# Optimization experiments

Measured on AMD Instinct MI355X. Metric: run time of the kernel, lower is better.

## Reference

```python
import jax, jax.numpy as jnp
import numpy as np

N, D, H = 500000, 128, 128
B, M = 1024, 512


def setup_inputs() -> dict:
    key = jax.random.key(0)
    k = jax.random.split(key, 8)
    return {
        "embed": jax.random.normal(k[0], (N, D), dtype=jnp.float32),
        "node_feat": jax.random.normal(k[1], (N, D), dtype=jnp.float32),
        "W1": jax.random.normal(k[2], (2 * D, H), dtype=jnp.float32) * 0.05,
        "b1": jnp.zeros((H,), dtype=jnp.float32),
        "W2": jax.random.normal(k[3], (H, 1), dtype=jnp.float32) * 0.05,
        "b2": jnp.zeros((1,), dtype=jnp.float32),
        "query_idx": jax.random.randint(k[4], (B,), 0, N),
        "cand_idx": jax.random.randint(k[5], (B, M), 0, N),
        "top_k": 3,
    }


def reference(embed, node_feat, W1, b1, W2, b2, query_idx, cand_idx, top_k):
    # Gather query and candidate (k-hop subgraph) embeddings.
    q = embed[query_idx]                                   # [B, D]
    c = embed[cand_idx]                                    # [B, M, D]
    Bv, Mv, Dv = c.shape
    pair = jnp.concatenate(
        [jnp.broadcast_to(q[:, None, :], (Bv, Mv, Dv)), c], axis=-1
    )                                                      # [B, M, 2D]
    # Tiny 2-layer MLP edge scorer (one fused pass over all edges).
    h = jax.nn.relu(jnp.einsum("bmf,fh->bmh", pair, W1) + b1)
    scores = (jnp.einsum("bmh,ho->bmo", h, W2) + b2)[..., 0]  # [B, M]
    # Sort-based top-k selection (original sorted per-etype lists).
    _, pos = jax.lax.top_k(scores, top_k)                  # [B, k]
    top_nodes = jnp.take_along_axis(cand_idx, pos, axis=1) # [B, k]
    # Zero out features of the selected nodes (hard mask), as in original.
    masked_feat = node_feat.at[top_nodes.reshape(-1)].set(0.0)
    return scores, masked_feat
```

## Files before the change

### kernel.cpp

```cpp
#include <hip/hip_runtime.h>
#include <math.h>

#define D 128
#define H 128
#define BQ 1024
#define M 512
#define NNODES 500000
#define K_MAX 8
#define SHORT 16
#define NTILE (BQ * M / 64)
#define NCOPY 2048
#define COPY_N4 ((long)NNODES * D / 4)

typedef __attribute__((ext_vector_type(8))) short bf16x8;
typedef __attribute__((ext_vector_type(4))) float f32x4;

static __device__ __forceinline__ unsigned pack2bf(float a, float b) {
    unsigned ua = __float_as_uint(a);
    unsigned ub = __float_as_uint(b);
    ua = ua + 0x7fffu + ((ua >> 16) & 1u);
    ub = ub + 0x7fffu + ((ub >> 16) & 1u);
    return (ua >> 16) | (ub & 0xffff0000u);
}

__global__ void wconv_kernel(const float* __restrict__ W1,
                             unsigned short* __restrict__ wTswz) {
    const int idx = blockIdx.x * 256 + threadIdx.x;
    const int h = idx >> 7;
    const int inner = (idx & 127) * 2;
    const int k = (inner ^ ((h & 7) << 4)) >> 1;
    const float v = W1[(long)(D + k) * H + h];
    wTswz[idx] = (unsigned short)pack2bf(v, 0.f);
}

__global__ void qproj_kernel(const float* __restrict__ embed,
                             const float* __restrict__ W1,
                             const float* __restrict__ b1,
                             const int* __restrict__ query_idx,
                             float* __restrict__ qh) {
    __shared__ float qrow[D];
    const int b = blockIdx.x;
    const int t = threadIdx.x;
    const long qi = query_idx[b];
    qrow[t] = embed[qi * D + t];
    __syncthreads();
    float acc = b1[t];
#pragma unroll 8
    for (int d = 0; d < D; ++d)
        acc = fmaf(qrow[d], W1[d * H + t], acc);
    qh[b * H + t] = acc;
}

__global__ __launch_bounds__(256)
void fused_kernel(const float* __restrict__ embed,
                  const unsigned short* __restrict__ wTswz,
                  const float* __restrict__ W2,
                  const float* __restrict__ b2,
                  const int* __restrict__ cand_idx,
                  const float* __restrict__ qh,
                  float* __restrict__ scores,
                  const f32x4* __restrict__ nf_src,
                  f32x4* __restrict__ nf_dst) {
    __shared__ __align__(16) char smem[16384 + 32768];
    const int bid = blockIdx.x;
    const int t   = threadIdx.x;

    if (bid % 5 == 0) {
        const int cb = bid / 5;
        long i = (long)cb * 256 + t;
        const long stride = (long)NCOPY * 256;
        for (; i < COPY_N4; i += stride) {
            const f32x4 v = __builtin_nontemporal_load(&nf_src[i]);
            __builtin_nontemporal_store(v, &nf_dst[i]);
        }
        return;
    }

    char* As = smem;
    char* Bs = smem + 16384;

    const int tile = bid - bid / 5 - 1;
    const int b   = tile >> 3;
    const int m0  = (tile & 7) * 64;

    {
        const int e = t >> 2;
        const int q = t & 3;
        const long node = cand_idx[b * M + m0 + e];
        const float* rowp = embed + node * D;
        const int sw = (e & 7) << 4;
#pragma unroll
        for (int i = 0; i < 8; ++i) {
            const int c4 = i * 4 + q;
            const f32x4 v = *(const f32x4*)(rowp + c4 * 4);
            uint2 p;
            p.x = pack2bf(v.x, v.y);
            p.y = pack2bf(v.z, v.w);
            *(uint2*)(As + (e << 8) + ((c4 * 8) ^ sw)) = p;
        }
    }
    {
#pragma unroll
        for (int i = 0; i < 8; ++i) {
            const int c = i * 256 + t;
            const uint4 v = ((const uint4*)wTswz)[c];
            *(uint4*)(Bs + (size_t)c * 16) = v;
        }
    }
    __syncthreads();

    const int lane = t & 63;
    const int w    = t >> 6;
    const int g    = lane >> 4;
    const int c    = lane & 15;
    const int sw   = (c & 7) << 4;

    f32x4 acc[8];
#pragma unroll
    for (int cb2 = 0; cb2 < 8; ++cb2) acc[cb2] = (f32x4){0.f, 0.f, 0.f, 0.f};

    const int arow = (w * 16 + c) << 8;
#pragma unroll
    for (int ks = 0; ks < 4; ++ks) {
        const int koff = (ks * 64 + g * 16) ^ sw;
        const bf16x8 a = *(const bf16x8*)(As + arow + koff);
#pragma unroll
        for (int cb2 = 0; cb2 < 8; ++cb2) {
            const bf16x8 bv = *(const bf16x8*)(Bs + ((cb2 * 16 + c) << 8) + koff);
            acc[cb2] = __builtin_amdgcn_mfma_f32_16x16x32_bf16(a, bv, acc[cb2], 0, 0, 0);
        }
    }

    float s0 = 0.f, s1 = 0.f, s2 = 0.f, s3 = 0.f;
#pragma unroll
    for (int cb2 = 0; cb2 < 8; ++cb2) {
        const int hq = cb2 * 16 + c;
        const float qv = qh[b * H + hq];
        const float w2 = W2[hq];
        s0 = fmaf(fmaxf(qv + acc[cb2][0], 0.f), w2, s0);
        s1 = fmaf(fmaxf(qv + acc[cb2][1], 0.f), w2, s1);
        s2 = fmaf(fmaxf(qv + acc[cb2][2], 0.f), w2, s2);
        s3 = fmaf(fmaxf(qv + acc[cb2][3], 0.f), w2, s3);
    }
#pragma unroll
    for (int off = 1; off <= 8; off <<= 1) {
        s0 += __shfl_xor(s0, off);
        s1 += __shfl_xor(s1, off);
        s2 += __shfl_xor(s2, off);
        s3 += __shfl_xor(s3, off);
    }
    if (c == 0) {
        const float b2v = b2[0];
        float* out = scores + b * M + m0 + w * 16 + g * 4;
        out[0] = s0 + b2v;
        out[1] = s1 + b2v;
        out[2] = s2 + b2v;
        out[3] = s3 + b2v;
    }
}

__global__ void topk16_kernel(const float* __restrict__ scores,
                              int* __restrict__ shortpos) {
    const int b = blockIdx.x;
    const int lane = threadIdx.x;
    const float* row = scores + b * M;
    float v[8];
    {
        const float4 x0 = ((const float4*)row)[lane * 2];
        const float4 x1 = ((const float4*)row)[lane * 2 + 1];
        v[0] = x0.x; v[1] = x0.y; v[2] = x0.z; v[3] = x0.w;
        v[4] = x1.x; v[5] = x1.y; v[6] = x1.z; v[7] = x1.w;
    }
    for (int kk = 0; kk < SHORT; ++kk) {
        float bv = v[0];
        int bi = lane * 8;
#pragma unroll
        for (int j = 1; j < 8; ++j)
            if (v[j] > bv) { bv = v[j]; bi = lane * 8 + j; }
#pragma unroll
        for (int off = 32; off >= 1; off >>= 1) {
            const float ov = __shfl_xor(bv, off);
            const int   oi = __shfl_xor(bi, off);
            if (ov > bv || (ov == bv && oi < bi)) { bv = ov; bi = oi; }
        }
        if (lane == 0) shortpos[b * SHORT + kk] = bi;
        if ((bi >> 3) == lane) v[bi & 7] = -3.402823466e38f;
    }
}

__global__ __launch_bounds__(128)
void refine_kernel(const float* __restrict__ embed,
                   const float* __restrict__ W1,
                   const float* __restrict__ W2,
                   const float* __restrict__ qh,
                   const int* __restrict__ cand_idx,
                   const int* __restrict__ shortpos,
                   const int* __restrict__ topk_ptr,
                   int* __restrict__ top_nodes) {
    __shared__ float crows[SHORT][D];
    __shared__ float red[SHORT][D];
    __shared__ int spos[SHORT];
    const int b = blockIdx.x;
    const int t = threadIdx.x;

    if (t < SHORT) spos[t] = shortpos[b * SHORT + t];
    __syncthreads();
    {
        const int cc = t >> 3;
        const int d0 = (t & 7) * 16;
        const long node = cand_idx[b * M + spos[cc]];
        const float4* rp = (const float4*)(embed + node * D);
        float4* wp = (float4*)&crows[cc][d0];
#pragma unroll
        for (int j = 0; j < 4; ++j) wp[j] = rp[d0 / 4 + j];
    }
    __syncthreads();

    float acc[SHORT];
#pragma unroll
    for (int cc = 0; cc < SHORT; ++cc) acc[cc] = 0.f;
    const float* W1bot = W1 + (long)D * H;
    for (int d = 0; d < D; ++d) {
        const float w1v = W1bot[d * H + t];
#pragma unroll
        for (int cc = 0; cc < SHORT; ++cc)
            acc[cc] = fmaf(crows[cc][d], w1v, acc[cc]);
    }
    const float qv = qh[b * H + t];
    const float w2 = W2[t];
#pragma unroll
    for (int cc = 0; cc < SHORT; ++cc)
        red[cc][t] = fmaxf(qv + acc[cc], 0.f) * w2;
    __syncthreads();

    if (t < 64) {
#pragma unroll
        for (int cc = 0; cc < SHORT; ++cc) {
            float v = red[cc][t] + red[cc][t + 64];
#pragma unroll
            for (int off = 32; off >= 1; off >>= 1) v += __shfl_xor(v, off);
            if (t == 0) red[cc][0] = v;
        }
    }
    __syncthreads();

    if (t == 0) {
        int k = *topk_ptr;
        if (k > K_MAX) k = K_MAX;
        unsigned used = 0;
        for (int kk = 0; kk < K_MAX; ++kk) {
            if (kk < k) {
                int best = -1, bpos = 0x7fffffff;
                float bv = 0.f;
                for (int cc = 0; cc < SHORT; ++cc) {
                    if (used & (1u << cc)) continue;
                    const float v = red[cc][0];
                    const int p = spos[cc];
                    if (best < 0 || v > bv || (v == bv && p < bpos)) {
                        best = cc; bv = v; bpos = p;
                    }
                }
                used |= 1u << best;
                top_nodes[b * K_MAX + kk] = cand_idx[b * M + bpos];
            } else {
                top_nodes[b * K_MAX + kk] = -1;
            }
        }
    }
}

__global__ void zero_rows_kernel(const int* __restrict__ top_nodes,
                                 float* __restrict__ masked) {
    const int node = top_nodes[blockIdx.x];
    if (node < 0) return;
    masked[(long)node * D + threadIdx.x] = 0.f;
}

extern "C" void kernel_launch(void* const* d_in, const int* in_sizes, int n_in,
                              void* d_out, int out_size, void* d_ws, size_t ws_size,
                              hipStream_t stream) {
    const float* embed     = (const float*)d_in[0];
    const float* node_feat = (const float*)d_in[1];
    const float* W1        = (const float*)d_in[2];
    const float* b1        = (const float*)d_in[3];
    const float* W2        = (const float*)d_in[4];
    const float* b2        = (const float*)d_in[5];
    const int*   query_idx = (const int*)d_in[6];
    const int*   cand_idx  = (const int*)d_in[7];
    const int*   topk_ptr  = (const int*)d_in[8];

    float* scores = (float*)d_out;
    float* masked = (float*)d_out + (long)BQ * M;

    char* p = (char*)d_ws;
    float*          qh        = (float*)p;          p += (long)BQ * H * 4;
    int*            shortpos  = (int*)p;            p += (long)BQ * SHORT * 4;
    int*            top_nodes = (int*)p;            p += (long)BQ * K_MAX * 4;
    unsigned short* wTswz     = (unsigned short*)p;

    wconv_kernel<<<(H * D) / 256, 256, 0, stream>>>(W1, wTswz);
    qproj_kernel<<<BQ, H, 0, stream>>>(embed, W1, b1, query_idx, qh);

    fused_kernel<<<NTILE + NCOPY, 256, 0, stream>>>(
        embed, wTswz, W2, b2, cand_idx, qh, scores,
        (const f32x4*)node_feat, (f32x4*)masked);

    topk16_kernel<<<BQ, 64, 0, stream>>>(scores, shortpos);
    refine_kernel<<<BQ, 128, 0, stream>>>(embed, W1, W2, qh, cand_idx,
                                          shortpos, topk_ptr, top_nodes);
    zero_rows_kernel<<<BQ * K_MAX, D, 0, stream>>>(top_nodes, masked);
}
```

Baseline: 205.6 us.

## Score one query per block with register-prefetched gathers and amortized W1 staging

```diff
diff --git a/kernel.cpp b/kernel.cpp
--- a/kernel.cpp
+++ b/kernel.cpp
@@ -8,12 +8,14 @@
 #define NNODES 500000
 #define K_MAX 8
 #define SHORT 16
-#define NTILE (BQ * M / 64)
+#define NSCORE BQ
 #define NCOPY 2048
 #define COPY_N4 ((long)NNODES * D / 4)
+#define CSTRIDE ((long)NCOPY * 256)
 
 typedef __attribute__((ext_vector_type(8))) short bf16x8;
 typedef __attribute__((ext_vector_type(4))) float f32x4;
+typedef __attribute__((ext_vector_type(4))) unsigned u32x4;
 
 static __device__ __forceinline__ unsigned pack2bf(float a, float b) {
     unsigned ua = __float_as_uint(a);
@@ -51,7 +53,7 @@
     qh[b * H + t] = acc;
 }
 
-__global__ __launch_bounds__(256)
+__global__ __launch_bounds__(256, 4)
 void fused_kernel(const float* __restrict__ embed,
                   const unsigned short* __restrict__ wTswz,
                   const float* __restrict__ W2,
@@ -61,44 +63,33 @@
                   float* __restrict__ scores,
                   const f32x4* __restrict__ nf_src,
                   f32x4* __restrict__ nf_dst) {
-    __shared__ __align__(16) char smem[16384 + 32768];
+    __shared__ __align__(16) char Bs[32768];
     const int bid = blockIdx.x;
     const int t   = threadIdx.x;
-
-    if (bid % 5 == 0) {
-        const int cb = bid / 5;
-        long i = (long)cb * 256 + t;
-        const long stride = (long)NCOPY * 256;
-        for (; i < COPY_N4; i += stride) {
+    const int r3  = bid % 3;
+
+    if (r3 != 1) {
+        const int cid = (bid / 3) * 2 + (r3 >> 1);
+        long i = (long)cid * 256 + t;
+        for (; i + 3 * CSTRIDE < COPY_N4; i += 4 * CSTRIDE) {
+            const f32x4 v0 = __builtin_nontemporal_load(&nf_src[i]);
+            const f32x4 v1 = __builtin_nontemporal_load(&nf_src[i + CSTRIDE]);
+            const f32x4 v2 = __builtin_nontemporal_load(&nf_src[i + 2 * CSTRIDE]);
+            const f32x4 v3 = __builtin_nontemporal_load(&nf_src[i + 3 * CSTRIDE]);
+            __builtin_nontemporal_store(v0, &nf_dst[i]);
+            __builtin_nontemporal_store(v1, &nf_dst[i + CSTRIDE]);
+            __builtin_nontemporal_store(v2, &nf_dst[i + 2 * CSTRIDE]);
+            __builtin_nontemporal_store(v3, &nf_dst[i + 3 * CSTRIDE]);
+        }
+        for (; i < COPY_N4; i += CSTRIDE) {
             const f32x4 v = __builtin_nontemporal_load(&nf_src[i]);
             __builtin_nontemporal_store(v, &nf_dst[i]);
         }
         return;
     }
 
-    char* As = smem;
-    char* Bs = smem + 16384;
-
-    const int tile = bid - bid / 5 - 1;
-    const int b   = tile >> 3;
-    const int m0  = (tile & 7) * 64;
-
-    {
-        const int e = t >> 2;
-        const int q = t & 3;
-        const long node = cand_idx[b * M + m0 + e];
-        const float* rowp = embed + node * D;
-        const int sw = (e & 7) << 4;
-#pragma unroll
-        for (int i = 0; i < 8; ++i) {
-            const int c4 = i * 4 + q;
-            const f32x4 v = *(const f32x4*)(rowp + c4 * 4);
-            uint2 p;
-            p.x = pack2bf(v.x, v.y);
-            p.y = pack2bf(v.z, v.w);
-            *(uint2*)(As + (e << 8) + ((c4 * 8) ^ sw)) = p;
-        }
-    }
+    const int b = bid / 3;
+
     {
 #pragma unroll
         for (int i = 0; i < 8; ++i) {
@@ -107,7 +98,6 @@
             *(uint4*)(Bs + (size_t)c * 16) = v;
         }
     }
-    __syncthreads();
 
     const int lane = t & 63;
     const int w    = t >> 6;
@@ -115,47 +105,87 @@
     const int c    = lane & 15;
     const int sw   = (c & 7) << 4;
 
-    f32x4 acc[8];
-#pragma unroll
-    for (int cb2 = 0; cb2 < 8; ++cb2) acc[cb2] = (f32x4){0.f, 0.f, 0.f, 0.f};
-
-    const int arow = (w * 16 + c) << 8;
-#pragma unroll
-    for (int ks = 0; ks < 4; ++ks) {
-        const int koff = (ks * 64 + g * 16) ^ sw;
-        const bf16x8 a = *(const bf16x8*)(As + arow + koff);
-#pragma unroll
-        for (int cb2 = 0; cb2 < 8; ++cb2) {
-            const bf16x8 bv = *(const bf16x8*)(Bs + ((cb2 * 16 + c) << 8) + koff);
-            acc[cb2] = __builtin_amdgcn_mfma_f32_16x16x32_bf16(a, bv, acc[cb2], 0, 0, 0);
-        }
-    }
-
-    float s0 = 0.f, s1 = 0.f, s2 = 0.f, s3 = 0.f;
-#pragma unroll
-    for (int cb2 = 0; cb2 < 8; ++cb2) {
-        const int hq = cb2 * 16 + c;
-        const float qv = qh[b * H + hq];
-        const float w2 = W2[hq];
-        s0 = fmaf(fmaxf(qv + acc[cb2][0], 0.f), w2, s0);
-        s1 = fmaf(fmaxf(qv + acc[cb2][1], 0.f), w2, s1);
-        s2 = fmaf(fmaxf(qv + acc[cb2][2], 0.f), w2, s2);
-        s3 = fmaf(fmaxf(qv + acc[cb2][3], 0.f), w2, s3);
-    }
-#pragma unroll
-    for (int off = 1; off <= 8; off <<= 1) {
-        s0 += __shfl_xor(s0, off);
-        s1 += __shfl_xor(s1, off);
-        s2 += __shfl_xor(s2, off);
-        s3 += __shfl_xor(s3, off);
-    }
-    if (c == 0) {
-        const float b2v = b2[0];
-        float* out = scores + b * M + m0 + w * 16 + g * 4;
-        out[0] = s0 + b2v;
-        out[1] = s1 + b2v;
-        out[2] = s2 + b2v;
-        out[3] = s3 + b2v;
+    float qv[8], w2[8];
+#pragma unroll
+    for (int cb = 0; cb < 8; ++cb) {
+        qv[cb] = qh[b * H + cb * 16 + c];
+        w2[cb] = W2[cb * 16 + c];
+    }
+    const float b2v = b2[0];
+
+    int idx[8];
+    const int ibase = b * M + w * 16 + c;
+#pragma unroll
+    for (int mt = 0; mt < 8; ++mt) idx[mt] = cand_idx[ibase + mt * 64];
+
+    __syncthreads();
+
+    f32x4 buf[8];
+    {
+        const float* rp = embed + (long)idx[0] * D + g * 8;
+#pragma unroll
+        for (int ks = 0; ks < 4; ++ks) {
+            buf[2 * ks]     = *(const f32x4*)(rp + ks * 32);
+            buf[2 * ks + 1] = *(const f32x4*)(rp + ks * 32 + 4);
+        }
+    }
+
+#pragma unroll
+    for (int mt = 0; mt < 8; ++mt) {
+        bf16x8 afr[4];
+#pragma unroll
+        for (int ks = 0; ks < 4; ++ks) {
+            u32x4 u;
+            u.x = pack2bf(buf[2 * ks].x, buf[2 * ks].y);
+            u.y = pack2bf(buf[2 * ks].z, buf[2 * ks].w);
+            u.z = pack2bf(buf[2 * ks + 1].x, buf[2 * ks + 1].y);
+            u.w = pack2bf(buf[2 * ks + 1].z, buf[2 * ks + 1].w);
+            afr[ks] = __builtin_bit_cast(bf16x8, u);
+        }
+        if (mt < 7) {
+            const float* rp = embed + (long)idx[mt + 1] * D + g * 8;
+#pragma unroll
+            for (int ks = 0; ks < 4; ++ks) {
+                buf[2 * ks]     = *(const f32x4*)(rp + ks * 32);
+                buf[2 * ks + 1] = *(const f32x4*)(rp + ks * 32 + 4);
+            }
+        }
+
+        f32x4 acc[8];
+#pragma unroll
+        for (int cb = 0; cb < 8; ++cb) acc[cb] = (f32x4){0.f, 0.f, 0.f, 0.f};
+#pragma unroll
+        for (int ks = 0; ks < 4; ++ks) {
+            const int koff = (ks * 64 + g * 16) ^ sw;
+#pragma unroll
+            for (int cb = 0; cb < 8; ++cb) {
+                const bf16x8 bv = *(const bf16x8*)(Bs + ((cb * 16 + c) << 8) + koff);
+                acc[cb] = __builtin_amdgcn_mfma_f32_16x16x32_bf16(afr[ks], bv, acc[cb], 0, 0, 0);
+            }
+        }
+
+        float s0 = 0.f, s1 = 0.f, s2 = 0.f, s3 = 0.f;
+#pragma unroll
+        for (int cb = 0; cb < 8; ++cb) {
+            s0 = fmaf(fmaxf(qv[cb] + acc[cb][0], 0.f), w2[cb], s0);
+            s1 = fmaf(fmaxf(qv[cb] + acc[cb][1], 0.f), w2[cb], s1);
+            s2 = fmaf(fmaxf(qv[cb] + acc[cb][2], 0.f), w2[cb], s2);
+            s3 = fmaf(fmaxf(qv[cb] + acc[cb][3], 0.f), w2[cb], s3);
+        }
+#pragma unroll
+        for (int off = 1; off <= 8; off <<= 1) {
+            s0 += __shfl_xor(s0, off);
+            s1 += __shfl_xor(s1, off);
+            s2 += __shfl_xor(s2, off);
+            s3 += __shfl_xor(s3, off);
+        }
+        if (c == 0) {
+            float* out = scores + b * M + mt * 64 + w * 16 + g * 4;
+            out[0] = s0 + b2v;
+            out[1] = s1 + b2v;
+            out[2] = s2 + b2v;
+            out[3] = s3 + b2v;
+        }
     }
 }
 
@@ -301,7 +331,7 @@
     wconv_kernel<<<(H * D) / 256, 256, 0, stream>>>(W1, wTswz);
     qproj_kernel<<<BQ, H, 0, stream>>>(embed, W1, b1, query_idx, qh);
 
-    fused_kernel<<<NTILE + NCOPY, 256, 0, stream>>>(
+    fused_kernel<<<NSCORE + NCOPY, 256, 0, stream>>>(
         embed, wTswz, W2, b2, cand_idx, qh, scores,
         (const f32x4*)node_feat, (f32x4*)masked);
 
```

Measured after the change: 182.6 us. 1.13x faster.
